# Performance work log

Hardware: AMD Instinct MI355X
Metric: run time of the kernel (lower is better)

Reference implementation:

```python
import jax, jax.numpy as jnp
import numpy as np

N_NODES = 100000
N_EDGES = 1600000
N_REL = 8
IN_CH = 16
HID_CH = 32
OUT_CH = 2


def setup_inputs() -> dict:
    key = jax.random.key(0)
    ks = jax.random.split(key, 9)
    x = jax.random.normal(ks[0], (N_NODES, IN_CH), dtype=jnp.float32)
    edge_index = jax.random.randint(ks[1], (2, N_EDGES), 0, N_NODES, dtype=jnp.int64)
    edge_type = jax.random.randint(ks[2], (N_EDGES,), 0, N_REL, dtype=jnp.int64)
    s = 0.1
    W1 = jax.random.normal(ks[3], (N_REL, IN_CH, HID_CH), dtype=jnp.float32) * s
    root1 = jax.random.normal(ks[4], (IN_CH, HID_CH), dtype=jnp.float32) * s
    b1 = jnp.zeros((HID_CH,), dtype=jnp.float32)
    W2 = jax.random.normal(ks[5], (N_REL, HID_CH, OUT_CH), dtype=jnp.float32) * s
    root2 = jax.random.normal(ks[6], (HID_CH, OUT_CH), dtype=jnp.float32) * s
    b2 = jnp.zeros((OUT_CH,), dtype=jnp.float32)
    return {"x": x, "edge_index": edge_index, "edge_type": edge_type,
            "W1": W1, "root1": root1, "b1": b1,
            "W2": W2, "root2": root2, "b2": b2}


def rgcn_conv(x, W, Wroot, b, src, dst, rel, num_nodes, num_rel):
    """PyG RGCNConv: per-relation mean aggregation + root weight + bias."""
    # Transform all nodes by all relation weights up front: [N, R, H]
    xW = jnp.einsum('nf,rfh->nrh', x, W)
    msg = xW[src, rel]                       # [E, H] gather per edge
    # mean per (dst, relation): normalize each message by its group size
    key = dst * num_rel + rel                # combined segment key
    ones = jnp.ones(rel.shape, dtype=x.dtype)
    cnt = jax.ops.segment_sum(ones, key, num_segments=num_nodes * num_rel)
    norm = 1.0 / jnp.maximum(cnt, 1.0)
    msg = msg * norm[key][:, None]
    agg = jax.ops.segment_sum(msg, dst, num_segments=num_nodes)  # sum over relations
    return agg + x @ Wroot + b


def reference(x, edge_index, edge_type, W1, root1, b1, W2, root2, b2):
    src, dst = edge_index[0], edge_index[1]
    h = rgcn_conv(x, W1, root1, b1, src, dst, edge_type, N_NODES, N_REL)
    h = jax.nn.relu(h)
    # dropout is identity in eval mode (training=False)
    out = rgcn_conv(h, W2, root2, b2, src, dst, edge_type, N_NODES, N_REL)
    return jax.nn.log_softmax(out, axis=1)
```

## Files before the change

### kernel.cpp

```cpp
#include <hip/hip_runtime.h>
#include <math.h>

#define N_REL  8
#define IN_CH  16
#define HID_CH 32
#define OUT_CH 2

#define BIN_BITS  9
#define BIN_NODES 512
#define KPB       (BIN_NODES * N_REL)
#define NCHUNK    192

static __device__ __forceinline__ unsigned short f2b(float f) {
    unsigned int u = __float_as_uint(f);
    u = (u + 0x7FFFu + ((u >> 16) & 1u)) >> 16;
    return (unsigned short)u;
}
static __device__ __forceinline__ float b2f(unsigned short s) {
    return __uint_as_float(((unsigned int)s) << 16);
}

__global__ __launch_bounds__(256) void part_hist_kernel(const int* __restrict__ dst,
                                                        int* __restrict__ H,
                                                        int E, int nbins, int chunksz) {
    __shared__ int hist[256];
    int chunk = blockIdx.x;
    int e0 = chunk * chunksz;
    int e1 = e0 + chunksz; if (e1 > E) e1 = E;

    for (int i = threadIdx.x; i < nbins; i += 256) hist[i] = 0;
    __syncthreads();
    for (int e = e0 + threadIdx.x; e < e1; e += 256)
        atomicAdd(&hist[dst[e] >> BIN_BITS], 1);
    __syncthreads();
    for (int i = threadIdx.x; i < nbins; i += 256)
        H[i * NCHUNK + chunk] = hist[i];
}

__global__ __launch_bounds__(1024) void scan_a_kernel(int* __restrict__ ptr,
                                                      int* __restrict__ blksum, int M) {
    int i = blockIdx.x * 1024 + threadIdx.x;
    int val = (i < M) ? ptr[i] : 0;
    int lane = threadIdx.x & 63;
    int wid  = threadIdx.x >> 6;

    int v = val;
#pragma unroll
    for (int off = 1; off < 64; off <<= 1) {
        int u = __shfl_up(v, off, 64);
        if (lane >= off) v += u;
    }

    __shared__ int wsum[16];
    if (lane == 63) wsum[wid] = v;
    __syncthreads();

    if (wid == 0) {
        int worig = (lane < 16) ? wsum[lane] : 0;
        int wv = worig;
#pragma unroll
        for (int off = 1; off < 16; off <<= 1) {
            int u = __shfl_up(wv, off, 64);
            if (lane >= off) wv += u;
        }
        if (lane < 16) wsum[lane] = wv - worig;
        if (lane == 15) blksum[blockIdx.x] = wv;
    }
    __syncthreads();

    if (i < M) ptr[i] = (v - val) + wsum[wid];
}

__global__ void scan_b_kernel(int* __restrict__ blksum, int nb) {
    int lane = threadIdx.x & 63;
    int run = 0;
    for (int base = 0; base < nb; base += 64) {
        int i = base + lane;
        int val = (i < nb) ? blksum[i] : 0;
        int v = val;
#pragma unroll
        for (int off = 1; off < 64; off <<= 1) {
            int u = __shfl_up(v, off, 64);
            if (lane >= off) v += u;
        }
        if (i < nb) blksum[i] = run + (v - val);
        run += __shfl(v, 63, 64);
    }
}

__global__ __launch_bounds__(1024) void scan_c_kernel(int* __restrict__ ptr,
                                                      const int* __restrict__ blksum, int M) {
    int i = blockIdx.x * 1024 + threadIdx.x;
    if (i < M) ptr[i] += blksum[blockIdx.x];
}

__global__ __launch_bounds__(256) void part_scatter_kernel(const int* __restrict__ src,
                                                           const int* __restrict__ dst,
                                                           const int* __restrict__ rel,
                                                           const int* __restrict__ Hs,
                                                           int* __restrict__ be,
                                                           int E, int nbins, int chunksz) {
    __shared__ int base[256];
    __shared__ int fil[256];
    int chunk = blockIdx.x;
    int e0 = chunk * chunksz;
    int e1 = e0 + chunksz; if (e1 > E) e1 = E;

    for (int i = threadIdx.x; i < nbins; i += 256) {
        base[i] = Hs[i * NCHUNK + chunk];
        fil[i]  = 0;
    }
    __syncthreads();

    for (int e = e0 + threadIdx.x; e < e1; e += 256) {
        int d = dst[e];
        int b = d >> BIN_BITS;
        int slot = base[b] + atomicAdd(&fil[b], 1);
        be[slot] = ((d & (BIN_NODES - 1)) << 20) | (rel[e] << 17) | src[e];
    }
}

__global__ __launch_bounds__(256) void bin_build_kernel(const int* __restrict__ be,
                                                        const int* __restrict__ Hs,
                                                        int* __restrict__ ends,
                                                        int* __restrict__ csr,
                                                        float* __restrict__ einv,
                                                        int E, int nbins) {
    int b  = blockIdx.x;
    int s0 = Hs[b * NCHUNK];
    int s1 = (b + 1 < nbins) ? Hs[(b + 1) * NCHUNK] : E;
    int t  = threadIdx.x;

    __shared__ int cnt[KPB];
    __shared__ int off[KPB];
    __shared__ int fil[KPB];
    __shared__ int ws[4];

    for (int i = t; i < KPB; i += 256) { cnt[i] = 0; fil[i] = 0; }
    __syncthreads();

    for (int p = s0 + t; p < s1; p += 256)
        atomicAdd(&cnt[be[p] >> 17], 1);
    __syncthreads();

    int kbase = t * 16;
    int loc[16];
    int sum = 0;
#pragma unroll
    for (int i = 0; i < 16; ++i) { loc[i] = sum; sum += cnt[kbase + i]; }

    int lane = t & 63, wid = t >> 6;
    int v = sum;
#pragma unroll
    for (int o = 1; o < 64; o <<= 1) {
        int u = __shfl_up(v, o, 64);
        if (lane >= o) v += u;
    }
    if (lane == 63) ws[wid] = v;
    __syncthreads();
    int woff = 0;
    for (int i = 0; i < wid; ++i) woff += ws[i];
    int excl = woff + (v - sum);
#pragma unroll
    for (int i = 0; i < 16; ++i) off[kbase + i] = excl + loc[i];
    __syncthreads();

    for (int i = t; i < KPB; i += 256)
        ends[b * KPB + i] = s0 + off[i] + cnt[i];

    for (int p = s0 + t; p < s1; p += 256) {
        int pk = be[p];
        int k  = pk >> 17;
        int slot = s0 + off[k] + atomicAdd(&fil[k], 1);
        csr[slot]  = ((pk & 0x1FFFF) << 3) | (k & 7);
        einv[slot] = 1.0f / (float)cnt[k];
    }
}

#define XW_TILE 64
__global__ __launch_bounds__(256) void xw_kernel(const float* __restrict__ x,
                                                 const float* __restrict__ W1,
                                                 unsigned short* __restrict__ xW16, int N) {
    __shared__ float sx[XW_TILE * IN_CH];
    int t = threadIdx.x;
    int node0 = blockIdx.x * XW_TILE;

    {
        int i4 = node0 * 4 + t;
        float4 v = make_float4(0.f, 0.f, 0.f, 0.f);
        if (i4 < N * 4) v = ((const float4*)x)[i4];
        ((float4*)sx)[t] = v;
    }
    __syncthreads();

    int r = t >> 5, c = t & 31;
    float w[IN_CH];
#pragma unroll
    for (int f = 0; f < IN_CH; ++f)
        w[f] = W1[(r * IN_CH + f) * HID_CH + c];

    int lim = N - node0; if (lim > XW_TILE) lim = XW_TILE;
    for (int ni = 0; ni < lim; ++ni) {
        const float4* xs = (const float4*)(sx + ni * IN_CH);
        float4 v0 = xs[0], v1 = xs[1], v2 = xs[2], v3 = xs[3];
        float a;
        a  = v0.x * w[0]  + v0.y * w[1]  + v0.z * w[2]  + v0.w * w[3];
        a += v1.x * w[4]  + v1.y * w[5]  + v1.z * w[6]  + v1.w * w[7];
        a += v2.x * w[8]  + v2.y * w[9]  + v2.z * w[10] + v2.w * w[11];
        a += v3.x * w[12] + v3.y * w[13] + v3.z * w[14] + v3.w * w[15];
        xW16[(node0 + ni) * (N_REL * HID_CH) + t] = f2b(a);
    }
}

#define STAGE_SW2(sw2, W2, root2)                                              \
    for (int i = threadIdx.x; i < 288; i += 256) {                             \
        int f = i / 9, j = i - f * 9;                                          \
        float a, bb;                                                           \
        if (j < 8) { a = W2[(j * HID_CH + f) * 2]; bb = W2[(j * HID_CH + f) * 2 + 1]; } \
        else       { a = root2[f * 2];             bb = root2[f * 2 + 1]; }    \
        sw2[i] = make_float2(a, bb);                                           \
    }

#define EPILOGUE_V2(sw2, hval, node, c, hW16, hroot, b2)                       \
    {                                                                          \
        int g  = (c >> 4) << 4;                                                \
        int jj = c & 15; if (jj > 8) jj = 8;                                   \
        float o0 = 0.0f, o1 = 0.0f;                                            \
        _Pragma("unroll")                                                      \
        for (int k = 0; k < 16; ++k) {                                         \
            float hf = __shfl(hval, g + k, 32);                                \
            float2 wv = sw2[(g + k) * 9 + jj];                                 \
            o0 = fmaf(hf, wv.x, o0);                                           \
            o1 = fmaf(hf, wv.y, o1);                                           \
        }                                                                      \
        o0 += __shfl_xor(o0, 16, 32);                                          \
        o1 += __shfl_xor(o1, 16, 32);                                          \
        if (c < 8) {                                                           \
            hW16[((node) << 3) + c] = ((unsigned)f2b(o1) << 16) | f2b(o0);     \
        } else if (c == 8) {                                                   \
            *(float2*)(hroot + ((long)(node) << 1)) =                          \
                make_float2(o0 + b2[0], o1 + b2[1]);                           \
        }                                                                      \
    }

__global__ __launch_bounds__(256) void l1_fused_kernel(const float* __restrict__ x,
                                                       const int* __restrict__ csr,
                                                       const float* __restrict__ einv,
                                                       const int* __restrict__ ends,
                                                       const unsigned short* __restrict__ xW16,
                                                       const float* __restrict__ root1,
                                                       const float* __restrict__ b1,
                                                       const float* __restrict__ W2,
                                                       const float* __restrict__ root2,
                                                       const float* __restrict__ b2,
                                                       unsigned int* __restrict__ hW16,
                                                       float* __restrict__ hroot, int N) {
    __shared__ float2 sw2[32 * 9];
    STAGE_SW2(sw2, W2, root2)
    __syncthreads();

    int gid  = blockIdx.x * 256 + threadIdx.x;
    int node = gid >> 5;
    int c    = gid & 31;
    if (node >= N) return;

    int p0 = (node > 0) ? __ldg(&ends[node * N_REL - 1]) : 0;
    int p1 = __ldg(&ends[node * N_REL + N_REL - 1]);

    float acc0 = 0.0f, acc1 = 0.0f;
    int p = p0;
    for (; p + 3 < p1; p += 4) {
        int v0 = csr[p], v1 = csr[p + 1], v2 = csr[p + 2], v3 = csr[p + 3];
        float i0 = einv[p], i1 = einv[p + 1], i2 = einv[p + 2], i3 = einv[p + 3];
        float a0 = b2f(xW16[(v0 << 5) + c]);
        float a1 = b2f(xW16[(v1 << 5) + c]);
        float a2 = b2f(xW16[(v2 << 5) + c]);
        float a3 = b2f(xW16[(v3 << 5) + c]);
        acc0 = fmaf(a0, i0, acc0);
        acc1 = fmaf(a1, i1, acc1);
        acc0 = fmaf(a2, i2, acc0);
        acc1 = fmaf(a3, i3, acc1);
    }
    if (p + 1 < p1) {
        int v0 = csr[p], v1 = csr[p + 1];
        float i0 = einv[p], i1 = einv[p + 1];
        acc0 = fmaf(b2f(xW16[(v0 << 5) + c]), i0, acc0);
        acc1 = fmaf(b2f(xW16[(v1 << 5) + c]), i1, acc1);
        p += 2;
    }
    if (p < p1)
        acc0 = fmaf(b2f(xW16[(csr[p] << 5) + c]), einv[p], acc0);

    const float4* xs = (const float4*)(x + ((long)node << 4));
    float4 v0 = xs[0], v1 = xs[1], v2 = xs[2], v3 = xs[3];
    const float* wr = root1 + c;
    float acc = acc0 + acc1 + b1[c];
    acc += v0.x * wr[0]   + v0.y * wr[32]  + v0.z * wr[64]  + v0.w * wr[96];
    acc += v1.x * wr[128] + v1.y * wr[160] + v1.z * wr[192] + v1.w * wr[224];
    acc += v2.x * wr[256] + v2.y * wr[288] + v2.z * wr[320] + v2.w * wr[352];
    acc += v3.x * wr[384] + v3.y * wr[416] + v3.z * wr[448] + v3.w * wr[480];
    float hval = fmaxf(acc, 0.0f);

    EPILOGUE_V2(sw2, hval, node, c, hW16, hroot, b2)
}

__global__ __launch_bounds__(256) void l1_fb_kernel(const float* __restrict__ x,
                                                    const int* __restrict__ csr,
                                                    const float* __restrict__ einv,
                                                    const int* __restrict__ ends,
                                                    const float* __restrict__ W1,
                                                    const float* __restrict__ root1,
                                                    const float* __restrict__ b1,
                                                    const float* __restrict__ W2,
                                                    const float* __restrict__ root2,
                                                    const float* __restrict__ b2,
                                                    unsigned int* __restrict__ hW16,
                                                    float* __restrict__ hroot, int N) {
    __shared__ float sW[N_REL * IN_CH * HID_CH];
    __shared__ float2 sw2[32 * 9];
    for (int i = threadIdx.x; i < N_REL * IN_CH * HID_CH; i += 256) sW[i] = W1[i];
    STAGE_SW2(sw2, W2, root2)
    __syncthreads();

    int gid  = blockIdx.x * 256 + threadIdx.x;
    int node = gid >> 5;
    int c    = gid & 31;
    if (node >= N) return;

    int p0 = (node > 0) ? __ldg(&ends[node * N_REL - 1]) : 0;
    int p1 = __ldg(&ends[node * N_REL + N_REL - 1]);

    float acc = 0.0f;
    for (int p = p0; p < p1; ++p) {
        int v = csr[p];
        int s = v >> 3, r = v & 7;
        const float4* xs = (const float4*)(x + ((long)s << 4));
        float4 q0 = xs[0], q1 = xs[1], q2 = xs[2], q3 = xs[3];
        const float* w = sW + ((r * IN_CH) * HID_CH) + c;
        float a;
        a  = q0.x * w[0]   + q0.y * w[32]  + q0.z * w[64]  + q0.w * w[96];
        a += q1.x * w[128] + q1.y * w[160] + q1.z * w[192] + q1.w * w[224];
        a += q2.x * w[256] + q2.y * w[288] + q2.z * w[320] + q2.w * w[352];
        a += q3.x * w[384] + q3.y * w[416] + q3.z * w[448] + q3.w * w[480];
        acc = fmaf(a, einv[p], acc);
    }

    const float4* xs = (const float4*)(x + ((long)node << 4));
    float4 v0 = xs[0], v1 = xs[1], v2 = xs[2], v3 = xs[3];
    const float* wr = root1 + c;
    acc += b1[c];
    acc += v0.x * wr[0]   + v0.y * wr[32]  + v0.z * wr[64]  + v0.w * wr[96];
    acc += v1.x * wr[128] + v1.y * wr[160] + v1.z * wr[192] + v1.w * wr[224];
    acc += v2.x * wr[256] + v2.y * wr[288] + v2.z * wr[320] + v2.w * wr[352];
    acc += v3.x * wr[384] + v3.y * wr[416] + v3.z * wr[448] + v3.w * wr[480];
    float hval = fmaxf(acc, 0.0f);

    EPILOGUE_V2(sw2, hval, node, c, hW16, hroot, b2)
}

__global__ __launch_bounds__(256) void l2_finish_kernel(const int* __restrict__ csr,
                                                        const int* __restrict__ ends,
                                                        const unsigned int* __restrict__ hW16,
                                                        const float* __restrict__ hroot,
                                                        float* __restrict__ out, int N) {
    int gid  = blockIdx.x * 256 + threadIdx.x;
    int node = gid >> 3;
    int r    = gid & 7;
    if (node >= N) return;

    int idx  = node * N_REL + r;
    int prev = (idx > 0) ? ends[idx - 1] : 0;
    int end  = ends[idx];

    float o0 = 0.0f, o1 = 0.0f;
    if (end > prev) {
        float s0 = 0.0f, s1 = 0.0f;
        int p = prev;
        for (; p + 1 < end; p += 2) {
            int a = csr[p] >> 3, b = csr[p + 1] >> 3;
            unsigned va = hW16[(a << 3) + r];
            unsigned vb = hW16[(b << 3) + r];
            s0 += b2f((unsigned short)va) + b2f((unsigned short)vb);
            s1 += b2f((unsigned short)(va >> 16)) + b2f((unsigned short)(vb >> 16));
        }
        if (p < end) {
            unsigned va = hW16[((csr[p] >> 3) << 3) + r];
            s0 += b2f((unsigned short)va);
            s1 += b2f((unsigned short)(va >> 16));
        }
        float inv = 1.0f / (float)(end - prev);
        o0 = s0 * inv; o1 = s1 * inv;
    }

#pragma unroll
    for (int m = 1; m < 8; m <<= 1) {
        o0 += __shfl_xor(o0, m, 64);
        o1 += __shfl_xor(o1, m, 64);
    }

    if (r == 0) {
        float2 rt = *(const float2*)(hroot + ((long)node << 1));
        o0 += rt.x; o1 += rt.y;
        float mx = fmaxf(o0, o1);
        float l  = mx + logf(__expf(o0 - mx) + __expf(o1 - mx));
        *(float2*)(out + ((long)node << 1)) = make_float2(o0 - l, o1 - l);
    }
}

extern "C" void kernel_launch(void* const* d_in, const int* in_sizes, int n_in,
                              void* d_out, int out_size, void* d_ws, size_t ws_size,
                              hipStream_t stream) {
    const float* x     = (const float*)d_in[0];
    const int*   eidx  = (const int*)d_in[1];
    const int*   etype = (const int*)d_in[2];
    const float* W1    = (const float*)d_in[3];
    const float* root1 = (const float*)d_in[4];
    const float* b1    = (const float*)d_in[5];
    const float* W2    = (const float*)d_in[6];
    const float* root2 = (const float*)d_in[7];
    const float* b2    = (const float*)d_in[8];
    float* out = (float*)d_out;

    const int N = in_sizes[0] / IN_CH;
    const int E = in_sizes[2];
    const int nbins   = (N + BIN_NODES - 1) >> BIN_BITS;
    const int chunksz = (E + NCHUNK - 1) / NCHUNK;
    const int M2      = nbins * NCHUNK;
    const int* src = eidx;
    const int* dst = eidx + E;

    char* wp = (char*)d_ws;
    auto take = [&](size_t bytes) {
        char* p = wp;
        wp += (bytes + 63) & ~(size_t)63;
        return p;
    };
    int*   H      = (int*)take((size_t)M2 * sizeof(int));
    int*   blksum = (int*)take(4096 * sizeof(int));
    int*   ends   = (int*)take((size_t)nbins * KPB * sizeof(int));
    int*   csr    = (int*)take((size_t)E * sizeof(int));
    float* einv   = (float*)take((size_t)E * sizeof(float));
    int*   be     = (int*)take((size_t)E * sizeof(int));
    unsigned int* hW16 = (unsigned int*)take((size_t)N * N_REL * sizeof(unsigned int));
    float* hroot  = (float*)take((size_t)N * 2 * sizeof(float));
    unsigned short* xW16 = (unsigned short*)take((size_t)N * N_REL * HID_CH * sizeof(unsigned short));
    bool use_xw = ((size_t)(wp - (char*)d_ws) <= ws_size);

    const int B = 256;
    const int nb = (M2 + 1023) / 1024;

    part_hist_kernel<<<NCHUNK, B, 0, stream>>>(dst, H, E, nbins, chunksz);
    scan_a_kernel<<<nb, 1024, 0, stream>>>(H, blksum, M2);
    scan_b_kernel<<<1, 64, 0, stream>>>(blksum, nb);
    scan_c_kernel<<<nb, 1024, 0, stream>>>(H, blksum, M2);
    part_scatter_kernel<<<NCHUNK, B, 0, stream>>>(src, dst, etype, H, be, E, nbins, chunksz);
    bin_build_kernel<<<nbins, B, 0, stream>>>(be, H, ends, csr, einv, E, nbins);

    if (use_xw) {
        xw_kernel<<<(N + XW_TILE - 1) / XW_TILE, B, 0, stream>>>(x, W1, xW16, N);
        l1_fused_kernel<<<(N * 32 + B - 1) / B, B, 0, stream>>>(
            x, csr, einv, ends, xW16, root1, b1, W2, root2, b2, hW16, hroot, N);
    } else {
        l1_fb_kernel<<<(N * 32 + B - 1) / B, B, 0, stream>>>(
            x, csr, einv, ends, W1, root1, b1, W2, root2, b2, hW16, hroot, N);
    }

    l2_finish_kernel<<<(N * 8 + B - 1) / B, B, 0, stream>>>(csr, ends, hW16, hroot, out, N);
}
```

Baseline: 174.4 us.

## Merge xw into histogram kernel, drop scan pass, flatten layer-2 gather

Combines the node transform and the edge histogram into one launch using disjoint block ranges. It removes the scan fix-up kernel by adding the block sums where offsets are read. The layer-1 gather loop is unrolled to 8 for more loads in flight. Layer 2 now walks all of a node's edges with 16 lanes using precomputed per-edge weights instead of one lane per relation. This trades fewer launches and better balance for extra reads of the weight array.

New measurement: 157.0 us. -10.0%, faster.

```diff
diff --git a/kernel.cpp b/kernel.cpp
--- a/kernel.cpp
+++ b/kernel.cpp
@@ -10,6 +10,7 @@
 #define BIN_NODES 512
 #define KPB       (BIN_NODES * N_REL)
 #define NCHUNK    192
+#define XW_TILE   64
 
 static __device__ __forceinline__ unsigned short f2b(float f) {
     unsigned int u = __float_as_uint(f);
@@ -20,21 +21,57 @@
     return __uint_as_float(((unsigned int)s) << 16);
 }
 
-__global__ __launch_bounds__(256) void part_hist_kernel(const int* __restrict__ dst,
-                                                        int* __restrict__ H,
-                                                        int E, int nbins, int chunksz) {
+__global__ __launch_bounds__(256) void prep_kernel(const float* __restrict__ x,
+                                                   const float* __restrict__ W1,
+                                                   unsigned short* __restrict__ xW16,
+                                                   const int* __restrict__ dst,
+                                                   int* __restrict__ H,
+                                                   int N, int E, int nbins,
+                                                   int chunksz, int nxw) {
+    __shared__ float sx[XW_TILE * IN_CH];
     __shared__ int hist[256];
-    int chunk = blockIdx.x;
-    int e0 = chunk * chunksz;
-    int e1 = e0 + chunksz; if (e1 > E) e1 = E;
-
-    for (int i = threadIdx.x; i < nbins; i += 256) hist[i] = 0;
-    __syncthreads();
-    for (int e = e0 + threadIdx.x; e < e1; e += 256)
-        atomicAdd(&hist[dst[e] >> BIN_BITS], 1);
-    __syncthreads();
-    for (int i = threadIdx.x; i < nbins; i += 256)
-        H[i * NCHUNK + chunk] = hist[i];
+    int t = threadIdx.x;
+
+    if ((int)blockIdx.x < nxw) {
+        int node0 = blockIdx.x * XW_TILE;
+        {
+            int i4 = node0 * 4 + t;
+            float4 v = make_float4(0.f, 0.f, 0.f, 0.f);
+            if (i4 < N * 4) v = ((const float4*)x)[i4];
+            ((float4*)sx)[t] = v;
+        }
+        __syncthreads();
+
+        int r = t >> 5, c = t & 31;
+        float w[IN_CH];
+#pragma unroll
+        for (int f = 0; f < IN_CH; ++f)
+            w[f] = W1[(r * IN_CH + f) * HID_CH + c];
+
+        int lim = N - node0; if (lim > XW_TILE) lim = XW_TILE;
+        for (int ni = 0; ni < lim; ++ni) {
+            const float4* xs = (const float4*)(sx + ni * IN_CH);
+            float4 v0 = xs[0], v1 = xs[1], v2 = xs[2], v3 = xs[3];
+            float a;
+            a  = v0.x * w[0]  + v0.y * w[1]  + v0.z * w[2]  + v0.w * w[3];
+            a += v1.x * w[4]  + v1.y * w[5]  + v1.z * w[6]  + v1.w * w[7];
+            a += v2.x * w[8]  + v2.y * w[9]  + v2.z * w[10] + v2.w * w[11];
+            a += v3.x * w[12] + v3.y * w[13] + v3.z * w[14] + v3.w * w[15];
+            xW16[(node0 + ni) * (N_REL * HID_CH) + t] = f2b(a);
+        }
+    } else {
+        int chunk = blockIdx.x - nxw;
+        int e0 = chunk * chunksz;
+        int e1 = e0 + chunksz; if (e1 > E) e1 = E;
+
+        for (int i = t; i < nbins; i += 256) hist[i] = 0;
+        __syncthreads();
+        for (int e = e0 + t; e < e1; e += 256)
+            atomicAdd(&hist[dst[e] >> BIN_BITS], 1);
+        __syncthreads();
+        for (int i = t; i < nbins; i += 256)
+            H[i * NCHUNK + chunk] = hist[i];
+    }
 }
 
 __global__ __launch_bounds__(1024) void scan_a_kernel(int* __restrict__ ptr,
@@ -88,16 +125,11 @@
     }
 }
 
-__global__ __launch_bounds__(1024) void scan_c_kernel(int* __restrict__ ptr,
-                                                      const int* __restrict__ blksum, int M) {
-    int i = blockIdx.x * 1024 + threadIdx.x;
-    if (i < M) ptr[i] += blksum[blockIdx.x];
-}
-
 __global__ __launch_bounds__(256) void part_scatter_kernel(const int* __restrict__ src,
                                                            const int* __restrict__ dst,
                                                            const int* __restrict__ rel,
                                                            const int* __restrict__ Hs,
+                                                           const int* __restrict__ blksum,
                                                            int* __restrict__ be,
                                                            int E, int nbins, int chunksz) {
     __shared__ int base[256];
@@ -107,7 +139,8 @@
     int e1 = e0 + chunksz; if (e1 > E) e1 = E;
 
     for (int i = threadIdx.x; i < nbins; i += 256) {
-        base[i] = Hs[i * NCHUNK + chunk];
+        int idx = i * NCHUNK + chunk;
+        base[i] = Hs[idx] + blksum[idx >> 10];
         fil[i]  = 0;
     }
     __syncthreads();
@@ -122,13 +155,19 @@
 
 __global__ __launch_bounds__(256) void bin_build_kernel(const int* __restrict__ be,
                                                         const int* __restrict__ Hs,
+                                                        const int* __restrict__ blksum,
                                                         int* __restrict__ ends,
                                                         int* __restrict__ csr,
                                                         float* __restrict__ einv,
                                                         int E, int nbins) {
     int b  = blockIdx.x;
-    int s0 = Hs[b * NCHUNK];
-    int s1 = (b + 1 < nbins) ? Hs[(b + 1) * NCHUNK] : E;
+    int i0 = b * NCHUNK;
+    int s0 = Hs[i0] + blksum[i0 >> 10];
+    int s1 = E;
+    if (b + 1 < nbins) {
+        int i1 = (b + 1) * NCHUNK;
+        s1 = Hs[i1] + blksum[i1 >> 10];
+    }
     int t  = threadIdx.x;
 
     __shared__ int cnt[KPB];
@@ -174,41 +213,6 @@
         int slot = s0 + off[k] + atomicAdd(&fil[k], 1);
         csr[slot]  = ((pk & 0x1FFFF) << 3) | (k & 7);
         einv[slot] = 1.0f / (float)cnt[k];
-    }
-}
-
-#define XW_TILE 64
-__global__ __launch_bounds__(256) void xw_kernel(const float* __restrict__ x,
-                                                 const float* __restrict__ W1,
-                                                 unsigned short* __restrict__ xW16, int N) {
-    __shared__ float sx[XW_TILE * IN_CH];
-    int t = threadIdx.x;
-    int node0 = blockIdx.x * XW_TILE;
-
-    {
-        int i4 = node0 * 4 + t;
-        float4 v = make_float4(0.f, 0.f, 0.f, 0.f);
-        if (i4 < N * 4) v = ((const float4*)x)[i4];
-        ((float4*)sx)[t] = v;
-    }
-    __syncthreads();
-
-    int r = t >> 5, c = t & 31;
-    float w[IN_CH];
-#pragma unroll
-    for (int f = 0; f < IN_CH; ++f)
-        w[f] = W1[(r * IN_CH + f) * HID_CH + c];
-
-    int lim = N - node0; if (lim > XW_TILE) lim = XW_TILE;
-    for (int ni = 0; ni < lim; ++ni) {
-        const float4* xs = (const float4*)(sx + ni * IN_CH);
-        float4 v0 = xs[0], v1 = xs[1], v2 = xs[2], v3 = xs[3];
-        float a;
-        a  = v0.x * w[0]  + v0.y * w[1]  + v0.z * w[2]  + v0.w * w[3];
-        a += v1.x * w[4]  + v1.y * w[5]  + v1.z * w[6]  + v1.w * w[7];
-        a += v2.x * w[8]  + v2.y * w[9]  + v2.z * w[10] + v2.w * w[11];
-        a += v3.x * w[12] + v3.y * w[13] + v3.z * w[14] + v3.w * w[15];
-        xW16[(node0 + ni) * (N_REL * HID_CH) + t] = f2b(a);
     }
 }
 
@@ -269,23 +273,40 @@
 
     float acc0 = 0.0f, acc1 = 0.0f;
     int p = p0;
-    for (; p + 3 < p1; p += 4) {
-        int v0 = csr[p], v1 = csr[p + 1], v2 = csr[p + 2], v3 = csr[p + 3];
-        float i0 = einv[p], i1 = einv[p + 1], i2 = einv[p + 2], i3 = einv[p + 3];
+    for (; p + 7 < p1; p += 8) {
+        int v0 = csr[p],     v1 = csr[p + 1], v2 = csr[p + 2], v3 = csr[p + 3];
+        int v4 = csr[p + 4], v5 = csr[p + 5], v6 = csr[p + 6], v7 = csr[p + 7];
+        float i0 = einv[p],     i1 = einv[p + 1], i2 = einv[p + 2], i3 = einv[p + 3];
+        float i4 = einv[p + 4], i5 = einv[p + 5], i6 = einv[p + 6], i7 = einv[p + 7];
         float a0 = b2f(xW16[(v0 << 5) + c]);
         float a1 = b2f(xW16[(v1 << 5) + c]);
         float a2 = b2f(xW16[(v2 << 5) + c]);
         float a3 = b2f(xW16[(v3 << 5) + c]);
+        float a4 = b2f(xW16[(v4 << 5) + c]);
+        float a5 = b2f(xW16[(v5 << 5) + c]);
+        float a6 = b2f(xW16[(v6 << 5) + c]);
+        float a7 = b2f(xW16[(v7 << 5) + c]);
         acc0 = fmaf(a0, i0, acc0);
         acc1 = fmaf(a1, i1, acc1);
         acc0 = fmaf(a2, i2, acc0);
         acc1 = fmaf(a3, i3, acc1);
+        acc0 = fmaf(a4, i4, acc0);
+        acc1 = fmaf(a5, i5, acc1);
+        acc0 = fmaf(a6, i6, acc0);
+        acc1 = fmaf(a7, i7, acc1);
+    }
+    for (; p + 3 < p1; p += 4) {
+        int v0 = csr[p], v1 = csr[p + 1], v2 = csr[p + 2], v3 = csr[p + 3];
+        float i0 = einv[p], i1 = einv[p + 1], i2 = einv[p + 2], i3 = einv[p + 3];
+        acc0 = fmaf(b2f(xW16[(v0 << 5) + c]), i0, acc0);
+        acc1 = fmaf(b2f(xW16[(v1 << 5) + c]), i1, acc1);
+        acc0 = fmaf(b2f(xW16[(v2 << 5) + c]), i2, acc0);
+        acc1 = fmaf(b2f(xW16[(v3 << 5) + c]), i3, acc1);
     }
     if (p + 1 < p1) {
         int v0 = csr[p], v1 = csr[p + 1];
-        float i0 = einv[p], i1 = einv[p + 1];
-        acc0 = fmaf(b2f(xW16[(v0 << 5) + c]), i0, acc0);
-        acc1 = fmaf(b2f(xW16[(v1 << 5) + c]), i1, acc1);
+        acc0 = fmaf(b2f(xW16[(v0 << 5) + c]), einv[p], acc0);
+        acc1 = fmaf(b2f(xW16[(v1 << 5) + c]), einv[p + 1], acc1);
         p += 2;
     }
     if (p < p1)
@@ -358,52 +379,41 @@
     EPILOGUE_V2(sw2, hval, node, c, hW16, hroot, b2)
 }
 
-__global__ __launch_bounds__(256) void l2_finish_kernel(const int* __restrict__ csr,
-                                                        const int* __restrict__ ends,
-                                                        const unsigned int* __restrict__ hW16,
-                                                        const float* __restrict__ hroot,
-                                                        float* __restrict__ out, int N) {
+__global__ __launch_bounds__(256) void l2_flat_kernel(const int* __restrict__ csr,
+                                                      const float* __restrict__ einv,
+                                                      const int* __restrict__ ends,
+                                                      const unsigned int* __restrict__ hW16,
+                                                      const float* __restrict__ hroot,
+                                                      float* __restrict__ out, int N) {
     int gid  = blockIdx.x * 256 + threadIdx.x;
-    int node = gid >> 3;
-    int r    = gid & 7;
+    int node = gid >> 4;
+    int l    = gid & 15;
     if (node >= N) return;
 
-    int idx  = node * N_REL + r;
-    int prev = (idx > 0) ? ends[idx - 1] : 0;
-    int end  = ends[idx];
+    int p0 = (node > 0) ? __ldg(&ends[node * N_REL - 1]) : 0;
+    int p1 = __ldg(&ends[node * N_REL + N_REL - 1]);
 
     float o0 = 0.0f, o1 = 0.0f;
-    if (end > prev) {
-        float s0 = 0.0f, s1 = 0.0f;
-        int p = prev;
-        for (; p + 1 < end; p += 2) {
-            int a = csr[p] >> 3, b = csr[p + 1] >> 3;
-            unsigned va = hW16[(a << 3) + r];
-            unsigned vb = hW16[(b << 3) + r];
-            s0 += b2f((unsigned short)va) + b2f((unsigned short)vb);
-            s1 += b2f((unsigned short)(va >> 16)) + b2f((unsigned short)(vb >> 16));
-        }
-        if (p < end) {
-            unsigned va = hW16[((csr[p] >> 3) << 3) + r];
-            s0 += b2f((unsigned short)va);
-            s1 += b2f((unsigned short)(va >> 16));
-        }
-        float inv = 1.0f / (float)(end - prev);
-        o0 = s0 * inv; o1 = s1 * inv;
-    }
-
-#pragma unroll
-    for (int m = 1; m < 8; m <<= 1) {
+    for (int p = p0 + l; p < p1; p += 16) {
+        int v = csr[p];
+        float w = einv[p];
+        unsigned u = hW16[v];
+        o0 = fmaf(b2f((unsigned short)u), w, o0);
+        o1 = fmaf(b2f((unsigned short)(u >> 16)), w, o1);
+    }
+
+#pragma unroll
+    for (int m = 1; m < 16; m <<= 1) {
         o0 += __shfl_xor(o0, m, 64);
         o1 += __shfl_xor(o1, m, 64);
     }
 
-    if (r == 0) {
+    if (l == 0) {
         float2 rt = *(const float2*)(hroot + ((long)node << 1));
         o0 += rt.x; o1 += rt.y;
         float mx = fmaxf(o0, o1);
-        float l  = mx + logf(__expf(o0 - mx) + __expf(o1 - mx));
-        *(float2*)(out + ((long)node << 1)) = make_float2(o0 - l, o1 - l);
+        float lg = mx + logf(__expf(o0 - mx) + __expf(o1 - mx));
+        *(float2*)(out + ((long)node << 1)) = make_float2(o0 - lg, o1 - lg);
     }
 }
 
@@ -448,16 +458,15 @@
 
     const int B = 256;
     const int nb = (M2 + 1023) / 1024;
-
-    part_hist_kernel<<<NCHUNK, B, 0, stream>>>(dst, H, E, nbins, chunksz);
+    const int nxw = use_xw ? (N + XW_TILE - 1) / XW_TILE : 0;
+
+    prep_kernel<<<nxw + NCHUNK, B, 0, stream>>>(x, W1, xW16, dst, H, N, E, nbins, chunksz, nxw);
     scan_a_kernel<<<nb, 1024, 0, stream>>>(H, blksum, M2);
     scan_b_kernel<<<1, 64, 0, stream>>>(blksum, nb);
-    scan_c_kernel<<<nb, 1024, 0, stream>>>(H, blksum, M2);
-    part_scatter_kernel<<<NCHUNK, B, 0, stream>>>(src, dst, etype, H, be, E, nbins, chunksz);
-    bin_build_kernel<<<nbins, B, 0, stream>>>(be, H, ends, csr, einv, E, nbins);
+    part_scatter_kernel<<<NCHUNK, B, 0, stream>>>(src, dst, etype, H, blksum, be, E, nbins, chunksz);
+    bin_build_kernel<<<nbins, B, 0, stream>>>(be, H, blksum, ends, csr, einv, E, nbins);
 
     if (use_xw) {
-        xw_kernel<<<(N + XW_TILE - 1) / XW_TILE, B, 0, stream>>>(x, W1, xW16, N);
         l1_fused_kernel<<<(N * 32 + B - 1) / B, B, 0, stream>>>(
             x, csr, einv, ends, xW16, root1, b1, W2, root2, b2, hW16, hroot, N);
     } else {
@@ -465,5 +474,5 @@
             x, csr, einv, ends, W1, root1, b1, W2, root2, b2, hW16, hroot, N);
     }
 
-    l2_finish_kernel<<<(N * 8 + B - 1) / B, B, 0, stream>>>(csr, ends, hW16, hroot, out, N);
-}
+    l2_flat_kernel<<<(N * 16 + B - 1) / B, B, 0, stream>>>(csr, einv, ends, hW16, hroot, out, N);
+}
```
